# Kernel optimization log

Hardware: AMD Instinct MI355X
Metric: run time of the kernel (lower is better)

The kernel has to match this reference:

```python
import jax, jax.numpy as jnp
import numpy as np

N_NODES = 100000
N_EDGES = 1600000
D_IN, D_HID, N_CLS = 256, 128, 47


def setup_inputs() -> dict:
    key = jax.random.key(0)
    k = jax.random.split(key, 5)
    x = jax.random.normal(k[0], (N_NODES, D_IN), dtype=jnp.float32)
    edge_index = jax.random.randint(k[1], (2, N_EDGES), 0, N_NODES, dtype=jnp.int64)
    W1 = jax.random.normal(k[2], (D_IN, D_HID), dtype=jnp.float32) * 0.05
    b1 = jnp.zeros((D_HID,), dtype=jnp.float32)
    W2 = jax.random.normal(k[3], (D_HID, N_CLS), dtype=jnp.float32) * 0.05
    b2 = jnp.zeros((N_CLS,), dtype=jnp.float32)
    return {"x": x, "edge_index": edge_index, "W1": W1, "b1": b1, "W2": W2, "b2": b2}


def _gcn_conv(x, W, b, src, dst, norm, n):
    # PyG GCNConv: linear transform, normalized scatter-add aggregation, bias after
    h = x @ W                                   # [N, D_out]
    msg = h[src] * norm[:, None]                # gather over edges [E', D_out]
    agg = jax.ops.segment_sum(msg, dst, num_segments=n)
    return agg + b


def reference(x, edge_index, W1, b1, W2, b2):
    n = x.shape[0]
    loop = jnp.arange(n, dtype=edge_index.dtype)
    src = jnp.concatenate([edge_index[0], loop])  # add self-loops
    dst = jnp.concatenate([edge_index[1], loop])
    # symmetric normalization D^-1/2 (A+I) D^-1/2 (degree = in-degree incl. self-loop)
    deg = jax.ops.segment_sum(jnp.ones_like(dst, dtype=x.dtype), dst, num_segments=n)
    dinv = jnp.where(deg > 0, jax.lax.rsqrt(deg), 0.0)
    norm = dinv[src] * dinv[dst]                 # [E']
    h1 = jax.nn.relu(_gcn_conv(x, W1, b1, src, dst, norm, n))
    # dropout with training=False is identity
    out = _gcn_conv(h1, W2, b2, src, dst, norm, n)
    return out
```

## Files before the change

kernel.cpp:

```cpp
#include <hip/hip_runtime.h>
#include <hip/hip_bf16.h>

#define DIN 256
#define DHID 128
#define NCLS 47
#define BSHIFT 9
#define BNODES 512
#define NPART 256
#define BCAPS 9216
#define CHUNKE 6400

typedef __attribute__((ext_vector_type(8))) short short8;
typedef __attribute__((ext_vector_type(4))) float f32x4;

__device__ __forceinline__ short f2bf(float f) {
    __bf16 b = (__bf16)f;
    return __builtin_bit_cast(short, b);
}
__device__ __forceinline__ float bfu(unsigned int u) {
    return __uint_as_float(u << 16);
}
__device__ __forceinline__ float bfh(unsigned int u) {
    return __uint_as_float(u & 0xffff0000u);
}

__global__ __launch_bounds__(256) void k_prep_hist(const float* __restrict__ W1,
                                                   const float* __restrict__ W2,
                                                   short* __restrict__ W1s,
                                                   short* __restrict__ W2s,
                                                   const int* __restrict__ dst,
                                                   int* __restrict__ ghist,
                                                   int E, int NB, int chunk) {
    __shared__ int lh[256];
    int blk = blockIdx.x, t = threadIdx.x;
    if (blk < 16) {
        int tid = blk * 256 + t;
        int frag = tid >> 6, lane = tid & 63;
        int kt = frag >> 3, nt = frag & 7;
        int quad = lane >> 4, col = lane & 15;
        #pragma unroll
        for (int j = 0; j < 8; ++j) {
            int k = kt * 32 + quad * 8 + j;
            W1s[(size_t)tid * 8 + j] = f2bf(W1[k * DHID + nt * 16 + col]);
        }
    } else if (blk < 20) {
        int tid = (blk - 16) * 256 + t;
        int frag = tid >> 6, lane = tid & 63;
        int kt = frag >> 2, nt = frag & 3;
        int quad = lane >> 4, col = lane & 15;
        int c = nt * 16 + col;
        #pragma unroll
        for (int j = 0; j < 8; ++j) {
            int k = kt * 32 + quad * 8 + j;
            float v = (c < NCLS) ? W2[k * NCLS + c] : 0.0f;
            W2s[(size_t)tid * 8 + j] = f2bf(v);
        }
    } else {
        int p = blk - 20;
        for (int i = t; i < NB; i += 256) lh[i] = 0;
        __syncthreads();
        int lo = p * chunk, hi = min(E, lo + chunk);
        for (int i = lo + t; i < hi; i += 256)
            atomicAdd(&lh[dst[i] >> BSHIFT], 1);
        __syncthreads();
        for (int i = t; i < NB; i += 256) ghist[p * NB + i] = lh[i];
    }
}

__global__ __launch_bounds__(256) void k_colscan(const int* __restrict__ ghist,
                                                 int* __restrict__ goff,
                                                 int* __restrict__ btot, int NB) {
    __shared__ int wsum[4];
    int b = blockIdx.x, t = threadIdx.x;
    int v = ghist[t * NB + b];
    int incl = v;
    int lane = t & 63, w = t >> 6;
    #pragma unroll
    for (int off = 1; off < 64; off <<= 1) {
        int u = __shfl_up(incl, off, 64);
        if (lane >= off) incl += u;
    }
    if (lane == 63) wsum[w] = incl;
    __syncthreads();
    int wadd = 0;
    for (int i = 0; i < w; ++i) wadd += wsum[i];
    goff[t * NB + b] = wadd + incl - v;
    if (t == 255) btot[b] = wadd + incl;
}

__device__ __forceinline__ void scan_btot(const int* __restrict__ btot, int NB,
                                          int* lbase, int* wsum) {
    int t = threadIdx.x;
    int v = (t < NB) ? btot[t] : 0;
    int incl = v;
    int lane = t & 63, w = t >> 6;
    #pragma unroll
    for (int off = 1; off < 64; off <<= 1) {
        int u = __shfl_up(incl, off, 64);
        if (lane >= off) incl += u;
    }
    if (lane == 63) wsum[w] = incl;
    __syncthreads();
    int wadd = 0;
    for (int i = 0; i < w; ++i) wadd += wsum[i];
    lbase[t] = wadd + incl - v;
    __syncthreads();
}

__global__ __launch_bounds__(256) void k_scatter(const int* __restrict__ src,
                                                 const int* __restrict__ dst,
                                                 const int* __restrict__ ghist,
                                                 const int* __restrict__ goff,
                                                 const int* __restrict__ btot,
                                                 unsigned int* __restrict__ bbuf,
                                                 int E, int NB, int chunk) {
    __shared__ unsigned int stage[CHUNKE];
    __shared__ int sdest[CHUNKE];
    __shared__ int lcur[256];
    __shared__ int gdst[256];
    __shared__ int wsum[4];

    int blk = blockIdx.x, t = threadIdx.x;

    scan_btot(btot, NB, gdst, wsum);

    int v = (t < NB) ? ghist[blk * NB + t] : 0;
    {
        int incl = v;
        int lane = t & 63, w = t >> 6;
        #pragma unroll
        for (int off = 1; off < 64; off <<= 1) {
            int u = __shfl_up(incl, off, 64);
            if (lane >= off) incl += u;
        }
        if (lane == 63) wsum[w] = incl;
        __syncthreads();
        int wadd = 0;
        for (int i = 0; i < w; ++i) wadd += wsum[i];
        int ex = wadd + incl - v;
        lcur[t] = ex;
        if (t < NB) gdst[t] += goff[blk * NB + t] - ex;
    }
    __syncthreads();

    int lo = blk * chunk, hi = min(E, lo + chunk), cnt = hi - lo;
    for (int i = lo + t; i < hi; i += 256) {
        int d = dst[i];
        int b = d >> BSHIFT;
        int slot = atomicAdd(&lcur[b], 1);
        stage[slot] = (unsigned int)src[i] | ((unsigned int)(d & (BNODES - 1)) << 17);
        sdest[slot] = gdst[b] + slot;
    }
    __syncthreads();
    for (int i = t; i < cnt; i += 256)
        bbuf[sdest[i]] = stage[i];
}

__global__ __launch_bounds__(256) void k_bsort(const int* __restrict__ btot,
                                               unsigned int* __restrict__ bbuf,
                                               int* __restrict__ degi,
                                               int* __restrict__ beg,
                                               float* __restrict__ dinv, int n, int NB) {
    __shared__ unsigned int stage[BCAPS];
    __shared__ int hist[BNODES];
    __shared__ int cur[BNODES];
    __shared__ int lbase[256];
    __shared__ int wsum[4];

    int b = blockIdx.x, t = threadIdx.x;
    scan_btot(btot, NB, lbase, wsum);
    int cnt = min(btot[b], BCAPS);
    int gbase = lbase[b];
    int node0 = b << BSHIFT;

    if (t < 128) { ((int2*)hist)[t] = (int2){0, 0}; ((int2*)hist)[t + 128] = (int2){0, 0}; }
    __syncthreads();

    for (int i = t; i < cnt; i += 256) {
        unsigned int p = bbuf[gbase + i];
        stage[i] = p;
        atomicAdd(&hist[p >> 17], 1);
    }
    __syncthreads();

    int v0 = hist[2 * t], v1 = hist[2 * t + 1];
    int s = v0 + v1;
    int incl = s;
    int lane = t & 63, w = t >> 6;
    #pragma unroll
    for (int off = 1; off < 64; off <<= 1) {
        int u = __shfl_up(incl, off, 64);
        if (lane >= off) incl += u;
    }
    if (lane == 63) wsum[w] = incl;
    __syncthreads();
    int wadd = 0;
    for (int i = 0; i < w; ++i) wadd += wsum[i];
    int ex = wadd + incl - s;
    cur[2 * t] = ex;
    cur[2 * t + 1] = ex + v0;
    int nodeA = node0 + 2 * t, nodeB = node0 + 2 * t + 1;
    if (nodeA < n) {
        degi[nodeA] = v0;
        beg[nodeA]  = gbase + ex;
        dinv[nodeA] = rsqrtf((float)(v0 + 1));
    }
    if (nodeB < n) {
        degi[nodeB] = v1;
        beg[nodeB]  = gbase + ex + v0;
        dinv[nodeB] = rsqrtf((float)(v1 + 1));
    }
    __syncthreads();

    for (int i = t; i < cnt; i += 256) {
        unsigned int p = stage[i];
        int slot = atomicAdd(&cur[p >> 17], 1);
        bbuf[gbase + slot] = p & 0x1FFFFu;
    }
}

__global__ __launch_bounds__(256) void k_gemm1_mfma(const float* __restrict__ x,
                                                    const short* __restrict__ W1s,
                                                    short* __restrict__ hb, int n) {
    __shared__ short lw[32768];
    {
        const uint4* g = (const uint4*)W1s;
        uint4* l = (uint4*)lw;
        for (int i = threadIdx.x; i < 4096; i += 256) l[i] = g[i];
    }
    __syncthreads();

    int wave = threadIdx.x >> 6, lane = threadIdx.x & 63;
    int quad = lane >> 4, lrow = lane & 15;
    long long rowbase = (long long)blockIdx.x * 128 + wave * 32;

    f32x4 acc[2][8];
    #pragma unroll
    for (int rt = 0; rt < 2; ++rt)
        #pragma unroll
        for (int nt = 0; nt < 8; ++nt) acc[rt][nt] = (f32x4){0.f, 0.f, 0.f, 0.f};

    const short8* lf = (const short8*)lw;

    #pragma unroll
    for (int kt = 0; kt < 8; ++kt) {
        int k0 = kt * 32 + quad * 8;
        short8 a[2];
        #pragma unroll
        for (int rt = 0; rt < 2; ++rt) {
            long long row = rowbase + rt * 16 + lrow;
            float4 v0 = {0.f,0.f,0.f,0.f}, v1 = {0.f,0.f,0.f,0.f};
            if (row < n) {
                const float* xp = x + row * DIN + k0;
                v0 = *(const float4*)xp;
                v1 = *(const float4*)(xp + 4);
            }
            short8 av;
            av[0] = f2bf(v0.x); av[1] = f2bf(v0.y); av[2] = f2bf(v0.z); av[3] = f2bf(v0.w);
            av[4] = f2bf(v1.x); av[5] = f2bf(v1.y); av[6] = f2bf(v1.z); av[7] = f2bf(v1.w);
            a[rt] = av;
        }
        #pragma unroll
        for (int nt = 0; nt < 8; ++nt) {
            short8 b = lf[(kt * 8 + nt) * 64 + lane];
            acc[0][nt] = __builtin_amdgcn_mfma_f32_16x16x32_bf16(a[0], b, acc[0][nt], 0, 0, 0);
            acc[1][nt] = __builtin_amdgcn_mfma_f32_16x16x32_bf16(a[1], b, acc[1][nt], 0, 0, 0);
        }
    }
    #pragma unroll
    for (int rt = 0; rt < 2; ++rt)
        #pragma unroll
        for (int nt = 0; nt < 8; ++nt)
            #pragma unroll
            for (int r = 0; r < 4; ++r) {
                long long row = rowbase + rt * 16 + quad * 4 + r;
                if (row < n) hb[row * DHID + nt * 16 + lrow] = f2bf(acc[rt][nt][r]);
            }
}

__global__ void k_gather1(const int* __restrict__ beg, const int* __restrict__ degi,
                          const int* __restrict__ ssrc, const float* __restrict__ dinv,
                          const unsigned int* __restrict__ hu, const float* __restrict__ b1,
                          unsigned int* __restrict__ h1u, int n) {
    int node = blockIdx.x * 4 + (threadIdx.x >> 6);
    int t = threadIdx.x & 63;
    if (node >= n) return;
    int cnt = degi[node];
    int bg  = beg[node];
    float ax = 0.f, ay = 0.f;
    int k = 0;
    for (; k + 8 <= cnt; k += 8) {
        int s[8]; float dv[8]; unsigned int u[8];
        #pragma unroll
        for (int j = 0; j < 8; ++j) s[j] = ssrc[bg + k + j];
        #pragma unroll
        for (int j = 0; j < 8; ++j) { dv[j] = dinv[s[j]]; u[j] = hu[(size_t)s[j] * 64 + t]; }
        #pragma unroll
        for (int j = 0; j < 8; ++j) { ax += dv[j] * bfu(u[j]); ay += dv[j] * bfh(u[j]); }
    }
    for (; k + 4 <= cnt; k += 4) {
        int s[4]; float dv[4]; unsigned int u[4];
        #pragma unroll
        for (int j = 0; j < 4; ++j) s[j] = ssrc[bg + k + j];
        #pragma unroll
        for (int j = 0; j < 4; ++j) { dv[j] = dinv[s[j]]; u[j] = hu[(size_t)s[j] * 64 + t]; }
        #pragma unroll
        for (int j = 0; j < 4; ++j) { ax += dv[j] * bfu(u[j]); ay += dv[j] * bfh(u[j]); }
    }
    for (; k < cnt; ++k) {
        int s = ssrc[bg + k];
        float ds = dinv[s];
        unsigned int u = hu[(size_t)s * 64 + t];
        ax += ds * bfu(u);
        ay += ds * bfh(u);
    }
    float di = dinv[node];
    unsigned int us = hu[(size_t)node * 64 + t];
    float2 bb = ((const float2*)b1)[t];
    float vx = di * ax + bfu(us) * di * di + bb.x;
    float vy = di * ay + bfh(us) * di * di + bb.y;
    vx = vx > 0.f ? vx : 0.f;
    vy = vy > 0.f ? vy : 0.f;
    unsigned int o = (unsigned int)(unsigned short)f2bf(vx)
                   | ((unsigned int)(unsigned short)f2bf(vy) << 16);
    h1u[(size_t)node * 64 + t] = o;
}

__global__ __launch_bounds__(256) void k_gemm2_mfma(const short* __restrict__ h1b,
                                                    const short* __restrict__ W2s,
                                                    short* __restrict__ h2b, int n) {
    __shared__ short lw[8192];
    {
        const uint4* g = (const uint4*)W2s;
        uint4* l = (uint4*)lw;
        for (int i = threadIdx.x; i < 1024; i += 256) l[i] = g[i];
    }
    __syncthreads();

    int wave = threadIdx.x >> 6, lane = threadIdx.x & 63;
    int quad = lane >> 4, lrow = lane & 15;
    long long row0 = (long long)blockIdx.x * 64 + wave * 16;

    f32x4 acc[4];
    #pragma unroll
    for (int nt = 0; nt < 4; ++nt) acc[nt] = (f32x4){0.f, 0.f, 0.f, 0.f};

    const short8* lf = (const short8*)lw;

    #pragma unroll
    for (int kt = 0; kt < 4; ++kt) {
        long long row = row0 + lrow;
        short8 a = (short8){0,0,0,0,0,0,0,0};
        if (row < n) a = *(const short8*)(h1b + row * DHID + kt * 32 + quad * 8);
        #pragma unroll
        for (int nt = 0; nt < 4; ++nt)
            acc[nt] = __builtin_amdgcn_mfma_f32_16x16x32_bf16(a, lf[(kt * 4 + nt) * 64 + lane], acc[nt], 0, 0, 0);
    }
    #pragma unroll
    for (int nt = 0; nt < 4; ++nt)
        #pragma unroll
        for (int r = 0; r < 4; ++r) {
            long long row = row0 + quad * 4 + r;
            if (row < n) h2b[row * 64 + nt * 16 + lrow] = f2bf(acc[nt][r]);
        }
}

__global__ void k_gather2(const int* __restrict__ beg, const int* __restrict__ degi,
                          const int* __restrict__ ssrc, const float* __restrict__ dinv,
                          const unsigned short* __restrict__ h2b, const float* __restrict__ b2,
                          float* __restrict__ out, int n) {
    int node = blockIdx.x * 4 + (threadIdx.x >> 6);
    int t = threadIdx.x & 63;
    if (node >= n) return;
    int cnt = degi[node];
    int bg  = beg[node];
    float acc = 0.f;
    int k = 0;
    for (; k + 8 <= cnt; k += 8) {
        int s[8]; float dv[8]; unsigned int u[8];
        #pragma unroll
        for (int j = 0; j < 8; ++j) s[j] = ssrc[bg + k + j];
        #pragma unroll
        for (int j = 0; j < 8; ++j) { dv[j] = dinv[s[j]]; u[j] = h2b[(size_t)s[j] * 64 + t]; }
        #pragma unroll
        for (int j = 0; j < 8; ++j) acc += dv[j] * bfu(u[j]);
    }
    for (; k + 4 <= cnt; k += 4) {
        int s[4]; float dv[4]; unsigned int u[4];
        #pragma unroll
        for (int j = 0; j < 4; ++j) s[j] = ssrc[bg + k + j];
        #pragma unroll
        for (int j = 0; j < 4; ++j) { dv[j] = dinv[s[j]]; u[j] = h2b[(size_t)s[j] * 64 + t]; }
        #pragma unroll
        for (int j = 0; j < 4; ++j) acc += dv[j] * bfu(u[j]);
    }
    for (; k < cnt; ++k) {
        int s = ssrc[bg + k];
        acc += dinv[s] * bfu((unsigned int)h2b[(size_t)s * 64 + t]);
    }
    if (t < NCLS) {
        float di = dinv[node];
        float self = bfu((unsigned int)h2b[(size_t)node * 64 + t]);
        out[(size_t)node * NCLS + t] = di * acc + self * di * di + b2[t];
    }
}

extern "C" void kernel_launch(void* const* d_in, const int* in_sizes, int n_in,
                              void* d_out, int out_size, void* d_ws, size_t ws_size,
                              hipStream_t stream) {
    const float* x  = (const float*)d_in[0];
    const int*   ei = (const int*)d_in[1];
    const float* W1 = (const float*)d_in[2];
    const float* b1 = (const float*)d_in[3];
    const float* W2 = (const float*)d_in[4];
    const float* b2 = (const float*)d_in[5];

    const int n = in_sizes[0] / DIN;
    const int E = in_sizes[1] / 2;
    const int* src = ei;
    const int* dst = ei + E;
    float* out = (float*)d_out;

    const int NB = (n + BNODES - 1) >> BSHIFT;
    const int chunk = (E + NPART - 1) / NPART;

    char* w = (char*)d_ws;
    int*   ghist = (int*)w;                    w += (size_t)NPART * NB * 4;
    int*   goff  = (int*)w;                    w += (size_t)NPART * NB * 4;
    int*   btot  = (int*)w;                    w += ((size_t)NB * 4 + 15) & ~15ull;
    int*   degi  = (int*)w;                    w += (size_t)n * 4;
    int*   beg   = (int*)w;                    w += (size_t)n * 4;
    float* dinv  = (float*)w;                  w += (size_t)n * 4;
    short* W1s   = (short*)w;                  w += (size_t)32768 * 2;
    short* W2s   = (short*)w;                  w += (size_t)8192 * 2;
    unsigned int* bbuf = (unsigned int*)w;     w += (size_t)E * 4;
    short* hb    = (short*)w;                  w += (size_t)n * DHID * 2;
    short* h1b   = (short*)w;                  w += (size_t)n * DHID * 2;
    short* h2b   = (short*)w;                  w += (size_t)n * 64 * 2;

    k_prep_hist<<<20 + NPART, 256, 0, stream>>>(W1, W2, W1s, W2s, dst, ghist, E, NB, chunk);
    k_colscan<<<NB, 256, 0, stream>>>(ghist, goff, btot, NB);
    k_scatter<<<NPART, 256, 0, stream>>>(src, dst, ghist, goff, btot, bbuf, E, NB, chunk);
    k_bsort<<<NB, 256, 0, stream>>>(btot, bbuf, degi, beg, dinv, n, NB);

    k_gemm1_mfma<<<(n + 127) / 128, 256, 0, stream>>>(x, W1s, hb, n);
    k_gather1<<<(n + 3) / 4, 256, 0, stream>>>(beg, degi, (const int*)bbuf, dinv,
                                               (const unsigned int*)hb, b1,
                                               (unsigned int*)h1b, n);

    k_gemm2_mfma<<<(n + 63) / 64, 256, 0, stream>>>(h1b, W2s, h2b, n);
    k_gather2<<<(n + 3) / 4, 256, 0, stream>>>(beg, degi, (const int*)bbuf, dinv,
                                               (const unsigned short*)h2b, b2, out, n);
}
```

Before: 404.9 us.

## Prescale features by dinv in GEMM epilogue and vectorize gathers with uint4 lanes

The GEMM epilogues now multiply each output row by dinv[row], so the gather kernels no longer load dinv[src] per edge and only scale by the destination's dinv. The gather kernels are restructured so sub-groups of a wave each load a 16-byte uint4 slice of a different neighbor row, covering several edges per iteration, and then reduce the partial sums across sub-groups with shuffles. This removes one dependent random load per edge and widens memory transactions. The cost is extra shuffle reductions, lanes that sit idle in the tail loop, and a little extra bf16 rounding from pre-scaling before quantization.

```diff
diff --git a/kernel.cpp b/kernel.cpp
--- a/kernel.cpp
+++ b/kernel.cpp
@@ -22,6 +22,16 @@
 }
 __device__ __forceinline__ float bfh(unsigned int u) {
     return __uint_as_float(u & 0xffff0000u);
+}
+__device__ __forceinline__ unsigned int pack2(float lo, float hi) {
+    return (unsigned int)(unsigned short)f2bf(lo)
+         | ((unsigned int)(unsigned short)f2bf(hi) << 16);
+}
+__device__ __forceinline__ void add8(float* a, uint4 v) {
+    a[0] += bfu(v.x); a[1] += bfh(v.x);
+    a[2] += bfu(v.y); a[3] += bfh(v.y);
+    a[4] += bfu(v.z); a[5] += bfh(v.z);
+    a[6] += bfu(v.w); a[7] += bfh(v.w);
 }
 
 __global__ __launch_bounds__(256) void k_prep_hist(const float* __restrict__ W1,
@@ -221,6 +231,7 @@
 
 __global__ __launch_bounds__(256) void k_gemm1_mfma(const float* __restrict__ x,
                                                     const short* __restrict__ W1s,
+                                                    const float* __restrict__ dinv,
                                                     short* __restrict__ hb, int n) {
     __shared__ short lw[32768];
     {
@@ -267,6 +278,14 @@
             acc[1][nt] = __builtin_amdgcn_mfma_f32_16x16x32_bf16(a[1], b, acc[1][nt], 0, 0, 0);
         }
     }
+    float dvv[2][4];
+    #pragma unroll
+    for (int rt = 0; rt < 2; ++rt)
+        #pragma unroll
+        for (int r = 0; r < 4; ++r) {
+            long long row = rowbase + rt * 16 + quad * 4 + r;
+            dvv[rt][r] = (row < n) ? dinv[row] : 0.f;
+        }
     #pragma unroll
     for (int rt = 0; rt < 2; ++rt)
         #pragma unroll
@@ -274,60 +293,79 @@
             #pragma unroll
             for (int r = 0; r < 4; ++r) {
                 long long row = rowbase + rt * 16 + quad * 4 + r;
-                if (row < n) hb[row * DHID + nt * 16 + lrow] = f2bf(acc[rt][nt][r]);
+                if (row < n) hb[row * DHID + nt * 16 + lrow] = f2bf(acc[rt][nt][r] * dvv[rt][r]);
             }
 }
 
-__global__ void k_gather1(const int* __restrict__ beg, const int* __restrict__ degi,
+__global__ __launch_bounds__(256) void k_gather1(const int* __restrict__ beg,
+                          const int* __restrict__ degi,
                           const int* __restrict__ ssrc, const float* __restrict__ dinv,
-                          const unsigned int* __restrict__ hu, const float* __restrict__ b1,
-                          unsigned int* __restrict__ h1u, int n) {
+                          const uint4* __restrict__ hb4, const float* __restrict__ b1,
+                          uint4* __restrict__ h1u4, int n) {
     int node = blockIdx.x * 4 + (threadIdx.x >> 6);
     int t = threadIdx.x & 63;
     if (node >= n) return;
     int cnt = degi[node];
     int bg  = beg[node];
-    float ax = 0.f, ay = 0.f;
+    int grp = t >> 4, sub = t & 15;
+
+    float a[8] = {0.f,0.f,0.f,0.f,0.f,0.f,0.f,0.f};
     int k = 0;
+    for (; k + 16 <= cnt; k += 16) {
+        int s[4];
+        #pragma unroll
+        for (int q = 0; q < 4; ++q) s[q] = ssrc[bg + k + q * 4 + grp];
+        uint4 v[4];
+        #pragma unroll
+        for (int q = 0; q < 4; ++q) v[q] = hb4[(size_t)s[q] * 16 + sub];
+        #pragma unroll
+        for (int q = 0; q < 4; ++q) add8(a, v[q]);
+    }
     for (; k + 8 <= cnt; k += 8) {
-        int s[8]; float dv[8]; unsigned int u[8];
-        #pragma unroll
-        for (int j = 0; j < 8; ++j) s[j] = ssrc[bg + k + j];
-        #pragma unroll
-        for (int j = 0; j < 8; ++j) { dv[j] = dinv[s[j]]; u[j] = hu[(size_t)s[j] * 64 + t]; }
-        #pragma unroll
-        for (int j = 0; j < 8; ++j) { ax += dv[j] * bfu(u[j]); ay += dv[j] * bfh(u[j]); }
-    }
-    for (; k + 4 <= cnt; k += 4) {
-        int s[4]; float dv[4]; unsigned int u[4];
-        #pragma unroll
-        for (int j = 0; j < 4; ++j) s[j] = ssrc[bg + k + j];
-        #pragma unroll
-        for (int j = 0; j < 4; ++j) { dv[j] = dinv[s[j]]; u[j] = hu[(size_t)s[j] * 64 + t]; }
-        #pragma unroll
-        for (int j = 0; j < 4; ++j) { ax += dv[j] * bfu(u[j]); ay += dv[j] * bfh(u[j]); }
-    }
-    for (; k < cnt; ++k) {
-        int s = ssrc[bg + k];
-        float ds = dinv[s];
-        unsigned int u = hu[(size_t)s * 64 + t];
-        ax += ds * bfu(u);
-        ay += ds * bfh(u);
-    }
-    float di = dinv[node];
-    unsigned int us = hu[(size_t)node * 64 + t];
-    float2 bb = ((const float2*)b1)[t];
-    float vx = di * ax + bfu(us) * di * di + bb.x;
-    float vy = di * ay + bfh(us) * di * di + bb.y;
-    vx = vx > 0.f ? vx : 0.f;
-    vy = vy > 0.f ? vy : 0.f;
-    unsigned int o = (unsigned int)(unsigned short)f2bf(vx)
-                   | ((unsigned int)(unsigned short)f2bf(vy) << 16);
-    h1u[(size_t)node * 64 + t] = o;
+        int s0 = ssrc[bg + k + grp], s1 = ssrc[bg + k + 4 + grp];
+        uint4 v0 = hb4[(size_t)s0 * 16 + sub];
+        uint4 v1 = hb4[(size_t)s1 * 16 + sub];
+        add8(a, v0); add8(a, v1);
+    }
+    for (; k < cnt; k += 4) {
+        int idx = k + grp;
+        if (idx < cnt) {
+            int s = ssrc[bg + idx];
+            add8(a, hb4[(size_t)s * 16 + sub]);
+        }
+    }
+    if (grp == 0) add8(a, hb4[(size_t)node * 16 + sub]);
+
+    #pragma unroll
+    for (int j = 0; j < 8; ++j) {
+        a[j] += __shfl_xor(a[j], 16);
+        a[j] += __shfl_xor(a[j], 32);
+    }
+
+    if (grp == 0) {
+        float di = dinv[node];
+        float4 bA = ((const float4*)b1)[sub * 2];
+        float4 bB = ((const float4*)b1)[sub * 2 + 1];
+        float v0 = fmaxf(di * a[0] + bA.x, 0.f);
+        float v1 = fmaxf(di * a[1] + bA.y, 0.f);
+        float v2 = fmaxf(di * a[2] + bA.z, 0.f);
+        float v3 = fmaxf(di * a[3] + bA.w, 0.f);
+        float v4 = fmaxf(di * a[4] + bB.x, 0.f);
+        float v5 = fmaxf(di * a[5] + bB.y, 0.f);
+        float v6 = fmaxf(di * a[6] + bB.z, 0.f);
+        float v7 = fmaxf(di * a[7] + bB.w, 0.f);
+        uint4 o;
+        o.x = pack2(v0, v1);
+        o.y = pack2(v2, v3);
+        o.z = pack2(v4, v5);
+        o.w = pack2(v6, v7);
+        h1u4[(size_t)node * 16 + sub] = o;
+    }
 }
 
 __global__ __launch_bounds__(256) void k_gemm2_mfma(const short* __restrict__ h1b,
                                                     const short* __restrict__ W2s,
+                                                    const float* __restrict__ dinv,
                                                     short* __restrict__ h2b, int n) {
     __shared__ short lw[8192];
     {
@@ -356,52 +394,64 @@
         for (int nt = 0; nt < 4; ++nt)
             acc[nt] = __builtin_amdgcn_mfma_f32_16x16x32_bf16(a, lf[(kt * 4 + nt) * 64 + lane], acc[nt], 0, 0, 0);
     }
+    float dvv[4];
+    #pragma unroll
+    for (int r = 0; r < 4; ++r) {
+        long long row = row0 + quad * 4 + r;
+        dvv[r] = (row < n) ? dinv[row] : 0.f;
+    }
     #pragma unroll
     for (int nt = 0; nt < 4; ++nt)
         #pragma unroll
         for (int r = 0; r < 4; ++r) {
             long long row = row0 + quad * 4 + r;
-            if (row < n) h2b[row * 64 + nt * 16 + lrow] = f2bf(acc[nt][r]);
-        }
-}
-
-__global__ void k_gather2(const int* __restrict__ beg, const int* __restrict__ degi,
+            if (row < n) h2b[row * 64 + nt * 16 + lrow] = f2bf(acc[nt][r] * dvv[r]);
+        }
+}
+
+__global__ __launch_bounds__(256) void k_gather2(const int* __restrict__ beg,
+                          const int* __restrict__ degi,
                           const int* __restrict__ ssrc, const float* __restrict__ dinv,
-                          const unsigned short* __restrict__ h2b, const float* __restrict__ b2,
+                          const uint4* __restrict__ h2b4, const float* __restrict__ b2,
                           float* __restrict__ out, int n) {
     int node = blockIdx.x * 4 + (threadIdx.x >> 6);
     int t = threadIdx.x & 63;
     if (node >= n) return;
     int cnt = degi[node];
     int bg  = beg[node];
-    float acc = 0.f;
+    int grp = t >> 3, sub = t & 7;
+
+    float a[8] = {0.f,0.f,0.f,0.f,0.f,0.f,0.f,0.f};
     int k = 0;
-    for (; k + 8 <= cnt; k += 8) {
-        int s[8]; float dv[8]; unsigned int u[8];
-        #pragma unroll
-        for (int j = 0; j < 8; ++j) s[j] = ssrc[bg + k + j];
-        #pragma unroll
-        for (int j = 0; j < 8; ++j) { dv[j] = dinv[s[j]]; u[j] = h2b[(size_t)s[j] * 64 + t]; }
-        #pragma unroll
-        for (int j = 0; j < 8; ++j) acc += dv[j] * bfu(u[j]);
-    }
-    for (; k + 4 <= cnt; k += 4) {
-        int s[4]; float dv[4]; unsigned int u[4];
-        #pragma unroll
-        for (int j = 0; j < 4; ++j) s[j] = ssrc[bg + k + j];
-        #pragma unroll
-        for (int j = 0; j < 4; ++j) { dv[j] = dinv[s[j]]; u[j] = h2b[(size_t)s[j] * 64 + t]; }
-        #pragma unroll
-        for (int j = 0; j < 4; ++j) acc += dv[j] * bfu(u[j]);
-    }
-    for (; k < cnt; ++k) {
-        int s = ssrc[bg + k];
-        acc += dinv[s] * bfu((unsigned int)h2b[(size_t)s * 64 + t]);
-    }
-    if (t < NCLS) {
+    for (; k + 16 <= cnt; k += 16) {
+        int s0 = ssrc[bg + k + grp], s1 = ssrc[bg + k + 8 + grp];
+        uint4 v0 = h2b4[(size_t)s0 * 8 + sub];
+        uint4 v1 = h2b4[(size_t)s1 * 8 + sub];
+        add8(a, v0); add8(a, v1);
+    }
+    for (; k < cnt; k += 8) {
+        int idx = k + grp;
+        if (idx < cnt) {
+            int s = ssrc[bg + idx];
+            add8(a, h2b4[(size_t)s * 8 + sub]);
+        }
+    }
+    if (grp == 0) add8(a, h2b4[(size_t)node * 8 + sub]);
+
+    #pragma unroll
+    for (int j = 0; j < 8; ++j) {
+        a[j] += __shfl_xor(a[j], 8);
+        a[j] += __shfl_xor(a[j], 16);
+        a[j] += __shfl_xor(a[j], 32);
+    }
+
+    if (grp == 0) {
         float di = dinv[node];
-        float self = bfu((unsigned int)h2b[(size_t)node * 64 + t]);
-        out[(size_t)node * NCLS + t] = di * acc + self * di * di + b2[t];
+        #pragma unroll
+        for (int j = 0; j < 8; ++j) {
+            int c = sub * 8 + j;
+            if (c < NCLS) out[(size_t)node * NCLS + c] = di * a[j] + b2[c];
+        }
     }
 }
 
@@ -443,12 +493,12 @@
     k_scatter<<<NPART, 256, 0, stream>>>(src, dst, ghist, goff, btot, bbuf, E, NB, chunk);
     k_bsort<<<NB, 256, 0, stream>>>(btot, bbuf, degi, beg, dinv, n, NB);
 
-    k_gemm1_mfma<<<(n + 127) / 128, 256, 0, stream>>>(x, W1s, hb, n);
+    k_gemm1_mfma<<<(n + 127) / 128, 256, 0, stream>>>(x, W1s, dinv, hb, n);
     k_gather1<<<(n + 3) / 4, 256, 0, stream>>>(beg, degi, (const int*)bbuf, dinv,
-                                               (const unsigned int*)hb, b1,
-                                               (unsigned int*)h1b, n);
-
-    k_gemm2_mfma<<<(n + 63) / 64, 256, 0, stream>>>(h1b, W2s, h2b, n);
+                                               (const uint4*)hb, b1,
+                                               (uint4*)h1b, n);
+
+    k_gemm2_mfma<<<(n + 63) / 64, 256, 0, stream>>>(h1b, W2s, dinv, h2b, n);
     k_gather2<<<(n + 3) / 4, 256, 0, stream>>>(beg, degi, (const int*)bbuf, dinv,
-                                               (const unsigned short*)h2b, b2, out, n);
-}
+                                               (const uint4*)h2b, b2, out, n);
+}
```

After: 417.8 us. 1.03x slower.
